# Performance work log

Hardware: AMD Instinct MI355X
Metric: run time of the kernel (lower is better)

The kernel has to match this reference:

```python
import jax, jax.numpy as jnp
import numpy as np

N_ATOMS = 100000
N_CRYSTALS = 2048
ATOM_FEA_DIM = 64
NUM_HEAD = 32


def setup_inputs() -> dict:
    key = jax.random.key(0)
    k1, k2, k3, k4, k5 = jax.random.split(key, 5)
    atom_feas = jax.random.normal(k1, (N_ATOMS, ATOM_FEA_DIM), dtype=jnp.float32)
    Wk = jax.random.normal(k2, (ATOM_FEA_DIM, NUM_HEAD), dtype=jnp.float32) / jnp.sqrt(ATOM_FEA_DIM).astype(jnp.float32)
    bk = jax.random.normal(k3, (NUM_HEAD,), dtype=jnp.float32) * 0.01
    atomic_numbers = jax.random.randint(k4, (N_ATOMS,), 0, 94, dtype=jnp.int64 if jax.config.jax_enable_x64 else jnp.int32)
    atom_owner = jnp.sort(jax.random.randint(k5, (N_ATOMS,), 0, N_CRYSTALS, dtype=jnp.int64 if jax.config.jax_enable_x64 else jnp.int32))
    return {"atom_feas": atom_feas, "Wk": Wk, "bk": bk,
            "atomic_numbers": atomic_numbers, "atom_owner": atom_owner}


def reference(atom_feas, Wk, bk, atomic_numbers, atom_owner):
    # per-atom attention logits: [N, H]
    w = atom_feas @ Wk + bk
    # numerically-stable per-graph softmax over the ragged atom axis
    seg_max = jax.ops.segment_max(w, atom_owner, num_segments=N_CRYSTALS)  # [G, H]
    e = jnp.exp(w - seg_max[atom_owner])                                   # [N, H]
    seg_sum = jax.ops.segment_sum(e, atom_owner, num_segments=N_CRYSTALS)  # [G, H]
    p = e / seg_sum[atom_owner]                                            # [N, H]
    # per-graph atom_fea.T @ weight: outer product per atom, segment-summed -> [G, D, H]
    crystal = jax.ops.segment_sum(atom_feas[:, :, None] * p[:, None, :],
                                  atom_owner, num_segments=N_CRYSTALS)
    return crystal.reshape(N_CRYSTALS, ATOM_FEA_DIM * NUM_HEAD)
```

## Files before the change

kernel.cpp:

```cpp
#include <hip/hip_runtime.h>

#define NC 2048
#define D 64
#define H 32

__global__ void bounds_kernel(const int* __restrict__ owner,
                              int* __restrict__ bounds, int n) {
    int i = blockIdx.x * blockDim.x + threadIdx.x;
    if (i >= n) return;
    int o  = owner[i];
    int op = (i == 0) ? -1 : owner[i - 1];
    for (int g = op + 1; g <= o; ++g) bounds[g] = i;
    if (i == n - 1)
        for (int g = o + 1; g <= NC; ++g) bounds[g] = n;
}

#define FPAD 68
__global__ __launch_bounds__(256) void logits_kernel(
    const float* __restrict__ atom_feas,
    const float* __restrict__ Wk,
    const float* __restrict__ bk,
    float* __restrict__ e_out,
    int n)
{
    __shared__ float fea_lds[64 * FPAD];
    __shared__ float wk_lds[D * H];
    __shared__ float bk_lds[H];

    const int tid  = threadIdx.x;
    const int base = blockIdx.x * 64;
    const int na   = min(64, n - base);

    for (int i = tid; i < D * H; i += 256) wk_lds[i] = Wk[i];
    if (tid < H) bk_lds[tid] = bk[tid];

    {
        const float4* src = (const float4*)(atom_feas + (size_t)base * D);
        const int nf4 = na * (D / 4);
        for (int i = tid; i < nf4; i += 256) {
            const int a = i >> 4, c = i & 15;
            *(float4*)(fea_lds + a * FPAD + c * 4) = src[i];
        }
    }
    __syncthreads();

    const int a  = tid >> 2;
    const int h0 = (tid & 3) * 8;
    if (a < na) {
        float acc[8];
        #pragma unroll
        for (int j = 0; j < 8; ++j) acc[j] = bk_lds[h0 + j];

        const float* fr = fea_lds + a * FPAD;
        #pragma unroll
        for (int k = 0; k < D; k += 4) {
            const float4 f = *(const float4*)(fr + k);
            #pragma unroll
            for (int r = 0; r < 4; ++r) {
                const float fv = (&f.x)[r];
                const float4 w0 = *(const float4*)(wk_lds + (k + r) * H + h0);
                const float4 w1 = *(const float4*)(wk_lds + (k + r) * H + h0 + 4);
                acc[0] += fv * w0.x; acc[1] += fv * w0.y;
                acc[2] += fv * w0.z; acc[3] += fv * w0.w;
                acc[4] += fv * w1.x; acc[5] += fv * w1.y;
                acc[6] += fv * w1.z; acc[7] += fv * w1.w;
            }
        }
        float4 e0, e1;
        e0.x = __expf(acc[0]); e0.y = __expf(acc[1]);
        e0.z = __expf(acc[2]); e0.w = __expf(acc[3]);
        e1.x = __expf(acc[4]); e1.y = __expf(acc[5]);
        e1.z = __expf(acc[6]); e1.w = __expf(acc[7]);
        float* dst = e_out + (size_t)(base + a) * H + h0;
        *(float4*)(dst)     = e0;
        *(float4*)(dst + 4) = e1;
    }
}

__global__ __launch_bounds__(256) void readout2_kernel(
    const float* __restrict__ atom_feas,
    const float* __restrict__ e_mat,
    const int* __restrict__ bounds,
    float* __restrict__ out)
{
    __shared__ float fea_lds[64 * D];
    __shared__ float e_lds[64 * H];

    const int g   = blockIdx.x;
    const int tid = threadIdx.x;
    const int h   = tid & 31;
    const int grp = tid >> 5;

    const int s = bounds[g];
    const int e = bounds[g + 1];

    float acc[8];
    #pragma unroll
    for (int j = 0; j < 8; ++j) acc[j] = 0.f;
    float ps = 0.f;

    for (int base = s; base < e; base += 64) {
        const int na = min(64, e - base);
        {
            const float4* fsrc = (const float4*)(atom_feas + (size_t)base * D);
            float4* fdst = (float4*)fea_lds;
            for (int i = tid; i < na * (D / 4); i += 256) fdst[i] = fsrc[i];
            const float4* esrc = (const float4*)(e_mat + (size_t)base * H);
            float4* edst = (float4*)e_lds;
            for (int i = tid; i < na * (H / 4); i += 256) edst[i] = esrc[i];
        }
        __syncthreads();

        for (int a = 0; a < na; ++a) {
            const float p = e_lds[a * H + h];
            ps += p;
            const float4 f0 = *(const float4*)(fea_lds + a * D + grp * 8);
            const float4 f1 = *(const float4*)(fea_lds + a * D + grp * 8 + 4);
            acc[0] += f0.x * p; acc[1] += f0.y * p;
            acc[2] += f0.z * p; acc[3] += f0.w * p;
            acc[4] += f1.x * p; acc[5] += f1.y * p;
            acc[6] += f1.z * p; acc[7] += f1.w * p;
        }
        __syncthreads();
    }

    const float inv = (ps > 0.f) ? 1.0f / ps : 0.f;
    float* og = out + (size_t)g * (D * H);
    #pragma unroll
    for (int j = 0; j < 8; ++j) og[(grp * 8 + j) * H + h] = acc[j] * inv;
}

#define CHUNK 64
__global__ __launch_bounds__(256) void fused_kernel(
    const float* __restrict__ atom_feas,
    const float* __restrict__ Wk,
    const float* __restrict__ bk,
    const int* __restrict__ owner,
    float* __restrict__ out,
    int n_atoms)
{
    __shared__ float fea_lds[CHUNK * D];
    __shared__ float w_lds[CHUNK * H];
    __shared__ float wk_lds[D * H];
    __shared__ float bk_lds[H];

    const int g   = blockIdx.x;
    const int tid = threadIdx.x;
    const int h   = tid & 31;
    const int grp = tid >> 5;

    for (int i = tid; i < D * H; i += 256) wk_lds[i] = Wk[i];
    if (tid < H) bk_lds[tid] = bk[tid];

    int lo = 0, hi = n_atoms;
    while (lo < hi) { int mid = (lo + hi) >> 1; if (owner[mid] < g) lo = mid + 1; else hi = mid; }
    const int seg_start = lo;
    hi = n_atoms;
    while (lo < hi) { int mid = (lo + hi) >> 1; if (owner[mid] < g + 1) lo = mid + 1; else hi = mid; }
    const int seg_end = lo;

    float acc[8];
    #pragma unroll
    for (int j = 0; j < 8; ++j) acc[j] = 0.f;
    float ps = 0.f;

    __syncthreads();

    for (int base = seg_start; base < seg_end; base += CHUNK) {
        const int na = min(CHUNK, seg_end - base);
        {
            const int nf4 = na * (D / 4);
            const float4* src = (const float4*)(atom_feas + (size_t)base * D);
            float4* dst = (float4*)fea_lds;
            for (int i = tid; i < nf4; i += 256) dst[i] = src[i];
        }
        __syncthreads();

        for (int pi = tid; pi < na * H; pi += 256) {
            const int a  = pi >> 5;
            const int hh = pi & 31;
            const float* fr = fea_lds + a * D;
            float wv = bk_lds[hh];
            #pragma unroll
            for (int k = 0; k < D; k += 4) {
                float4 f = *(const float4*)(fr + k);
                wv += f.x * wk_lds[(k + 0) * H + hh];
                wv += f.y * wk_lds[(k + 1) * H + hh];
                wv += f.z * wk_lds[(k + 2) * H + hh];
                wv += f.w * wk_lds[(k + 3) * H + hh];
            }
            w_lds[pi] = __expf(wv);
        }
        __syncthreads();

        for (int a = 0; a < na; ++a) {
            const float p = w_lds[a * H + h];
            ps += p;
            const float* f = fea_lds + a * D + grp * 8;
            #pragma unroll
            for (int j = 0; j < 8; ++j) acc[j] += f[j] * p;
        }
        __syncthreads();
    }

    const float inv = (ps > 0.f) ? 1.0f / ps : 0.f;
    float* og = out + (size_t)g * (D * H);
    #pragma unroll
    for (int j = 0; j < 8; ++j) og[(grp * 8 + j) * H + h] = acc[j] * inv;
}

extern "C" void kernel_launch(void* const* d_in, const int* in_sizes, int n_in,
                              void* d_out, int out_size, void* d_ws, size_t ws_size,
                              hipStream_t stream) {
    const float* atom_feas = (const float*)d_in[0];
    const float* Wk        = (const float*)d_in[1];
    const float* bk        = (const float*)d_in[2];
    const int*   owner     = (const int*)d_in[4];
    const int n_atoms = in_sizes[4];
    float* out = (float*)d_out;

    const size_t bounds_bytes = 16384;
    const size_t e_bytes = (size_t)n_atoms * H * sizeof(float);

    if (ws_size >= bounds_bytes + e_bytes) {
        int*   bounds = (int*)d_ws;
        float* e_mat  = (float*)((char*)d_ws + bounds_bytes);

        bounds_kernel<<<(n_atoms + 255) / 256, 256, 0, stream>>>(owner, bounds, n_atoms);
        logits_kernel<<<(n_atoms + 63) / 64, 256, 0, stream>>>(atom_feas, Wk, bk, e_mat, n_atoms);
        readout2_kernel<<<NC, 256, 0, stream>>>(atom_feas, e_mat, bounds, out);
    } else {
        fused_kernel<<<NC, 256, 0, stream>>>(atom_feas, Wk, bk, owner, out, n_atoms);
    }
}
```

Before: 43.01 us.

## Fuse bounds into register-tiled logits kernel and register-accumulate readout

Folds the segment-bounds computation into the logits kernel, which removes one kernel launch. The logits kernel now stages features transposed in LDS and has each thread compute a 4x4 atom-by-head register tile. The readout kernel drops the LDS staging and block barriers: two waves stride over the segment's atoms, each lane accumulating an 8x4 outer-product tile in registers with a one-step prefetch. The two waves' partial sums are combined through LDS at the end. The trade-off is fewer threads per crystal and higher register pressure in exchange for less synchronisation and less LDS traffic.

```diff
diff --git a/kernel.cpp b/kernel.cpp
--- a/kernel.cpp
+++ b/kernel.cpp
@@ -3,131 +3,175 @@
 #define NC 2048
 #define D 64
 #define H 32
-
-__global__ void bounds_kernel(const int* __restrict__ owner,
-                              int* __restrict__ bounds, int n) {
-    int i = blockIdx.x * blockDim.x + threadIdx.x;
-    if (i >= n) return;
-    int o  = owner[i];
-    int op = (i == 0) ? -1 : owner[i - 1];
-    for (int g = op + 1; g <= o; ++g) bounds[g] = i;
-    if (i == n - 1)
-        for (int g = o + 1; g <= NC; ++g) bounds[g] = n;
-}
-
-#define FPAD 68
-__global__ __launch_bounds__(256) void logits_kernel(
+#define AB 128
+
+__global__ __launch_bounds__(256) void logits_bounds_kernel(
     const float* __restrict__ atom_feas,
     const float* __restrict__ Wk,
     const float* __restrict__ bk,
+    const int* __restrict__ owner,
     float* __restrict__ e_out,
+    int* __restrict__ bounds,
     int n)
 {
-    __shared__ float fea_lds[64 * FPAD];
+    __shared__ float fea_t[D][AB];
     __shared__ float wk_lds[D * H];
     __shared__ float bk_lds[H];
 
     const int tid  = threadIdx.x;
-    const int base = blockIdx.x * 64;
-    const int na   = min(64, n - base);
-
-    for (int i = tid; i < D * H; i += 256) wk_lds[i] = Wk[i];
+    const int base = blockIdx.x * AB;
+    const int na   = min(AB, n - base);
+
+    const int gi = blockIdx.x * 256 + tid;
+    if (gi < n) {
+        const int o  = owner[gi];
+        const int op = (gi == 0) ? -1 : owner[gi - 1];
+        for (int g = op + 1; g <= o; ++g) bounds[g] = gi;
+        if (gi == n - 1)
+            for (int g = o + 1; g <= NC; ++g) bounds[g] = n;
+    }
+
+    for (int i = tid; i < D * H / 4; i += 256)
+        ((float4*)wk_lds)[i] = ((const float4*)Wk)[i];
     if (tid < H) bk_lds[tid] = bk[tid];
 
-    {
-        const float4* src = (const float4*)(atom_feas + (size_t)base * D);
-        const int nf4 = na * (D / 4);
-        for (int i = tid; i < nf4; i += 256) {
-            const int a = i >> 4, c = i & 15;
-            *(float4*)(fea_lds + a * FPAD + c * 4) = src[i];
+    for (int i = tid; i < AB * (D / 4); i += 256) {
+        const int a  = i & (AB - 1);
+        const int kg = i >> 7;
+        if (a < na) {
+            const float4 f = *(const float4*)(atom_feas + (size_t)(base + a) * D + kg * 4);
+            fea_t[kg * 4 + 0][a] = f.x;
+            fea_t[kg * 4 + 1][a] = f.y;
+            fea_t[kg * 4 + 2][a] = f.z;
+            fea_t[kg * 4 + 3][a] = f.w;
         }
     }
     __syncthreads();
 
-    const int a  = tid >> 2;
-    const int h0 = (tid & 3) * 8;
-    if (a < na) {
-        float acc[8];
-        #pragma unroll
-        for (int j = 0; j < 8; ++j) acc[j] = bk_lds[h0 + j];
-
-        const float* fr = fea_lds + a * FPAD;
-        #pragma unroll
-        for (int k = 0; k < D; k += 4) {
-            const float4 f = *(const float4*)(fr + k);
-            #pragma unroll
-            for (int r = 0; r < 4; ++r) {
-                const float fv = (&f.x)[r];
-                const float4 w0 = *(const float4*)(wk_lds + (k + r) * H + h0);
-                const float4 w1 = *(const float4*)(wk_lds + (k + r) * H + h0 + 4);
-                acc[0] += fv * w0.x; acc[1] += fv * w0.y;
-                acc[2] += fv * w0.z; acc[3] += fv * w0.w;
-                acc[4] += fv * w1.x; acc[5] += fv * w1.y;
-                acc[6] += fv * w1.z; acc[7] += fv * w1.w;
-            }
-        }
-        float4 e0, e1;
-        e0.x = __expf(acc[0]); e0.y = __expf(acc[1]);
-        e0.z = __expf(acc[2]); e0.w = __expf(acc[3]);
-        e1.x = __expf(acc[4]); e1.y = __expf(acc[5]);
-        e1.z = __expf(acc[6]); e1.w = __expf(acc[7]);
-        float* dst = e_out + (size_t)(base + a) * H + h0;
-        *(float4*)(dst)     = e0;
-        *(float4*)(dst + 4) = e1;
-    }
-}
-
-__global__ __launch_bounds__(256) void readout2_kernel(
+    const int ag = tid >> 3;
+    const int hg = tid & 7;
+    const int a0 = ag * 4;
+    const int h0 = hg * 4;
+
+    float acc[4][4];
+    #pragma unroll
+    for (int j = 0; j < 4; ++j) {
+        #pragma unroll
+        for (int c = 0; c < 4; ++c) acc[j][c] = bk_lds[h0 + c];
+    }
+
+    #pragma unroll 8
+    for (int k = 0; k < D; ++k) {
+        const float4 wv = *(const float4*)(wk_lds + k * H + h0);
+        const float4 fv = *(const float4*)(&fea_t[k][a0]);
+        acc[0][0] += fv.x * wv.x; acc[0][1] += fv.x * wv.y; acc[0][2] += fv.x * wv.z; acc[0][3] += fv.x * wv.w;
+        acc[1][0] += fv.y * wv.x; acc[1][1] += fv.y * wv.y; acc[1][2] += fv.y * wv.z; acc[1][3] += fv.y * wv.w;
+        acc[2][0] += fv.z * wv.x; acc[2][1] += fv.z * wv.y; acc[2][2] += fv.z * wv.z; acc[2][3] += fv.z * wv.w;
+        acc[3][0] += fv.w * wv.x; acc[3][1] += fv.w * wv.y; acc[3][2] += fv.w * wv.z; acc[3][3] += fv.w * wv.w;
+    }
+
+    #pragma unroll
+    for (int j = 0; j < 4; ++j) {
+        if (a0 + j < na) {
+            float4 e4;
+            e4.x = __expf(acc[j][0]);
+            e4.y = __expf(acc[j][1]);
+            e4.z = __expf(acc[j][2]);
+            e4.w = __expf(acc[j][3]);
+            *(float4*)(e_out + (size_t)(base + a0 + j) * H + h0) = e4;
+        }
+    }
+}
+
+__global__ __launch_bounds__(128) void readout3_kernel(
     const float* __restrict__ atom_feas,
     const float* __restrict__ e_mat,
     const int* __restrict__ bounds,
     float* __restrict__ out)
 {
-    __shared__ float fea_lds[64 * D];
-    __shared__ float e_lds[64 * H];
-
-    const int g   = blockIdx.x;
-    const int tid = threadIdx.x;
-    const int h   = tid & 31;
-    const int grp = tid >> 5;
+    __shared__ float part[H * 64];
+    __shared__ float part_s[4 * 64];
+
+    const int g    = blockIdx.x;
+    const int tid  = threadIdx.x;
+    const int lane = tid & 63;
+    const int wid  = tid >> 6;
+    const int dg   = lane >> 3;
+    const int hg   = lane & 7;
+    const int d0   = dg * 8;
+    const int h0   = hg * 4;
 
     const int s = bounds[g];
     const int e = bounds[g + 1];
 
-    float acc[8];
-    #pragma unroll
-    for (int j = 0; j < 8; ++j) acc[j] = 0.f;
-    float ps = 0.f;
-
-    for (int base = s; base < e; base += 64) {
-        const int na = min(64, e - base);
+    float acc[8][4];
+    #pragma unroll
+    for (int j = 0; j < 8; ++j) {
+        #pragma unroll
+        for (int c = 0; c < 4; ++c) acc[j][c] = 0.f;
+    }
+    float es[4] = {0.f, 0.f, 0.f, 0.f};
+
+    int a = s + wid;
+    float4 f0, f1, e4;
+    if (a < e) {
+        f0 = *(const float4*)(atom_feas + (size_t)a * D + d0);
+        f1 = *(const float4*)(atom_feas + (size_t)a * D + d0 + 4);
+        e4 = *(const float4*)(e_mat + (size_t)a * H + h0);
+    }
+    while (a < e) {
+        const int an = a + 2;
+        float4 nf0, nf1, ne4;
+        if (an < e) {
+            nf0 = *(const float4*)(atom_feas + (size_t)an * D + d0);
+            nf1 = *(const float4*)(atom_feas + (size_t)an * D + d0 + 4);
+            ne4 = *(const float4*)(e_mat + (size_t)an * H + h0);
+        }
+        es[0] += e4.x; es[1] += e4.y; es[2] += e4.z; es[3] += e4.w;
         {
-            const float4* fsrc = (const float4*)(atom_feas + (size_t)base * D);
-            float4* fdst = (float4*)fea_lds;
-            for (int i = tid; i < na * (D / 4); i += 256) fdst[i] = fsrc[i];
-            const float4* esrc = (const float4*)(e_mat + (size_t)base * H);
-            float4* edst = (float4*)e_lds;
-            for (int i = tid; i < na * (H / 4); i += 256) edst[i] = esrc[i];
-        }
-        __syncthreads();
-
-        for (int a = 0; a < na; ++a) {
-            const float p = e_lds[a * H + h];
-            ps += p;
-            const float4 f0 = *(const float4*)(fea_lds + a * D + grp * 8);
-            const float4 f1 = *(const float4*)(fea_lds + a * D + grp * 8 + 4);
-            acc[0] += f0.x * p; acc[1] += f0.y * p;
-            acc[2] += f0.z * p; acc[3] += f0.w * p;
-            acc[4] += f1.x * p; acc[5] += f1.y * p;
-            acc[6] += f1.z * p; acc[7] += f1.w * p;
-        }
-        __syncthreads();
-    }
-
-    const float inv = (ps > 0.f) ? 1.0f / ps : 0.f;
-    float* og = out + (size_t)g * (D * H);
-    #pragma unroll
-    for (int j = 0; j < 8; ++j) og[(grp * 8 + j) * H + h] = acc[j] * inv;
+            const float fj0 = f0.x, fj1 = f0.y, fj2 = f0.z, fj3 = f0.w;
+            const float fj4 = f1.x, fj5 = f1.y, fj6 = f1.z, fj7 = f1.w;
+            acc[0][0] += fj0 * e4.x; acc[0][1] += fj0 * e4.y; acc[0][2] += fj0 * e4.z; acc[0][3] += fj0 * e4.w;
+            acc[1][0] += fj1 * e4.x; acc[1][1] += fj1 * e4.y; acc[1][2] += fj1 * e4.z; acc[1][3] += fj1 * e4.w;
+            acc[2][0] += fj2 * e4.x; acc[2][1] += fj2 * e4.y; acc[2][2] += fj2 * e4.z; acc[2][3] += fj2 * e4.w;
+            acc[3][0] += fj3 * e4.x; acc[3][1] += fj3 * e4.y; acc[3][2] += fj3 * e4.z; acc[3][3] += fj3 * e4.w;
+            acc[4][0] += fj4 * e4.x; acc[4][1] += fj4 * e4.y; acc[4][2] += fj4 * e4.z; acc[4][3] += fj4 * e4.w;
+            acc[5][0] += fj5 * e4.x; acc[5][1] += fj5 * e4.y; acc[5][2] += fj5 * e4.z; acc[5][3] += fj5 * e4.w;
+            acc[6][0] += fj6 * e4.x; acc[6][1] += fj6 * e4.y; acc[6][2] += fj6 * e4.z; acc[6][3] += fj6 * e4.w;
+            acc[7][0] += fj7 * e4.x; acc[7][1] += fj7 * e4.y; acc[7][2] += fj7 * e4.z; acc[7][3] += fj7 * e4.w;
+        }
+        f0 = nf0; f1 = nf1; e4 = ne4;
+        a = an;
+    }
+
+    if (wid == 1) {
+        #pragma unroll
+        for (int j = 0; j < 8; ++j) {
+            #pragma unroll
+            for (int c = 0; c < 4; ++c)
+                part[(j * 4 + c) * 64 + lane] = acc[j][c];
+        }
+        #pragma unroll
+        for (int c = 0; c < 4; ++c) part_s[c * 64 + lane] = es[c];
+    }
+    __syncthreads();
+    if (wid == 0) {
+        #pragma unroll
+        for (int c = 0; c < 4; ++c) es[c] += part_s[c * 64 + lane];
+        float inv[4];
+        #pragma unroll
+        for (int c = 0; c < 4; ++c) inv[c] = (es[c] > 0.f) ? 1.0f / es[c] : 0.f;
+        float* og = out + (size_t)g * (D * H);
+        #pragma unroll
+        for (int j = 0; j < 8; ++j) {
+            float4 o4;
+            o4.x = (acc[j][0] + part[(j * 4 + 0) * 64 + lane]) * inv[0];
+            o4.y = (acc[j][1] + part[(j * 4 + 1) * 64 + lane]) * inv[1];
+            o4.z = (acc[j][2] + part[(j * 4 + 2) * 64 + lane]) * inv[2];
+            o4.w = (acc[j][3] + part[(j * 4 + 3) * 64 + lane]) * inv[3];
+            *(float4*)(og + (d0 + j) * H + h0) = o4;
+        }
+    }
 }
 
 #define CHUNK 64
@@ -226,9 +270,10 @@
         int*   bounds = (int*)d_ws;
         float* e_mat  = (float*)((char*)d_ws + bounds_bytes);
 
-        bounds_kernel<<<(n_atoms + 255) / 256, 256, 0, stream>>>(owner, bounds, n_atoms);
-        logits_kernel<<<(n_atoms + 63) / 64, 256, 0, stream>>>(atom_feas, Wk, bk, e_mat, n_atoms);
-        readout2_kernel<<<NC, 256, 0, stream>>>(atom_feas, e_mat, bounds, out);
+        const int nb = (n_atoms + AB - 1) / AB;
+        logits_bounds_kernel<<<nb, 256, 0, stream>>>(atom_feas, Wk, bk, owner,
+                                                     e_mat, bounds, n_atoms);
+        readout3_kernel<<<NC, 128, 0, stream>>>(atom_feas, e_mat, bounds, out);
     } else {
         fused_kernel<<<NC, 256, 0, stream>>>(atom_feas, Wk, bk, owner, out, n_atoms);
     }
```

Result: faster. 38.87 us (-9.6%).
